# Optimization experiments

Hardware: AMD Instinct MI355X
Metric: run time of the kernel (lower is better)

## Reference

```python
import jax, jax.numpy as jnp
import numpy as np

B, T, C, H = 8, 1024, 768, 12
HD = C // H
EPS = 1e-5
NEG = jnp.finfo(jnp.float32).min


def layer_norm(x, scale, bias):
    mu = jnp.mean(x, axis=-1, keepdims=True)
    var = jnp.mean(jnp.square(x - mu), axis=-1, keepdims=True)
    return (x - mu) * jax.lax.rsqrt(var + EPS) * scale + bias


def setup_inputs() -> dict:
    key = jax.random.key(0)
    ks = jax.random.split(key, 8)
    s = lambda fan_in: 1.0 / np.sqrt(fan_in)
    x = jax.random.normal(ks[0], (B, T, C), dtype=jnp.float32)
    mask = jnp.tril(jnp.ones((T, T), dtype=bool))[None, None, :, :]
    return {
        "x": x,
        "mask": mask,
        "ln1_scale": jnp.ones((C,), jnp.float32),
        "ln1_bias": jnp.zeros((C,), jnp.float32),
        "w_qkv": jax.random.normal(ks[1], (C, 3 * C), jnp.float32) * s(C),
        "b_qkv": jnp.zeros((3 * C,), jnp.float32),
        "w_attn_proj": jax.random.normal(ks[2], (C, C), jnp.float32) * s(C),
        "b_attn_proj": jnp.zeros((C,), jnp.float32),
        "ln2_scale": jnp.ones((C,), jnp.float32),
        "ln2_bias": jnp.zeros((C,), jnp.float32),
        "w_fc": jax.random.normal(ks[3], (C, 4 * C), jnp.float32) * s(C),
        "b_fc": jnp.zeros((4 * C,), jnp.float32),
        "w_mlp_proj": jax.random.normal(ks[4], (4 * C, C), jnp.float32) * s(4 * C),
        "b_mlp_proj": jnp.zeros((C,), jnp.float32),
    }


def reference(x, mask, ln1_scale, ln1_bias, w_qkv, b_qkv, w_attn_proj,
              b_attn_proj, ln2_scale, ln2_bias, w_fc, b_fc, w_mlp_proj,
              b_mlp_proj):
    # --- attention branch (pre-LN) ---
    h = layer_norm(x, ln1_scale, ln1_bias)
    qkv = jnp.einsum('btc,cd->btd', h, w_qkv) + b_qkv      # [B,T,3C]
    qkv = qkv.reshape(B, T, 3 * H, HD)
    q, k, v = jnp.array_split(qkv, 3, axis=2)              # each [B,T,H,HD]
    scale = 1.0 / jnp.sqrt(jnp.float32(HD))
    attn = jnp.einsum('bqhd,bkhd->bhqk', q, k) * scale     # [B,H,T,T]
    attn = jnp.where(mask, attn, NEG)
    attn = jax.nn.softmax(attn, axis=-1)
    ctx = jnp.einsum('bhqk,bkhd->bqhd', attn, v).reshape(B, T, C)
    attn_out = jnp.einsum('btc,cd->btd', ctx, w_attn_proj) + b_attn_proj
    x = x + attn_out
    # --- MLP branch (pre-LN) ---
    h = layer_norm(x, ln2_scale, ln2_bias)
    h = jax.nn.gelu(jnp.einsum('btc,cf->btf', h, w_fc) + b_fc)  # tanh approx, as flax default
    mlp_out = jnp.einsum('btf,fc->btc', h, w_mlp_proj) + b_mlp_proj
    return x + mlp_out
```

## Files before the change

### kernel.cpp

```cpp
#include <hip/hip_runtime.h>
#include <hip/hip_bf16.h>
#include <cstdint>
#include <math.h>

#define BB 8
#define TT 1024
#define CC 768
#define HH 12
#define MROWS (BB*TT)

typedef __hip_bfloat16 bf16;
typedef __attribute__((ext_vector_type(8))) __bf16 bf16x8;
typedef __attribute__((ext_vector_type(4))) float f32x4;

#define MFMA16(a,b,c) __builtin_amdgcn_mfma_f32_16x16x32_bf16(a,b,c,0,0,0)

__device__ __forceinline__ void lds_barrier() {
  asm volatile("s_waitcnt lgkmcnt(0)\n\ts_barrier" ::: "memory");
}

__global__ __launch_bounds__(256) void ln_kernel(
    const float* __restrict__ x, const float* __restrict__ scale,
    const float* __restrict__ bias, bf16* __restrict__ out)
{
  int row = blockIdx.x;
  const float* xr = x + (size_t)row * CC;
  float v[3];
  float s = 0.f, s2 = 0.f;
  for (int i = 0; i < 3; i++) {
    v[i] = xr[threadIdx.x + i*256];
    s += v[i]; s2 += v[i]*v[i];
  }
  for (int m = 1; m < 64; m <<= 1) { s += __shfl_xor(s, m); s2 += __shfl_xor(s2, m); }
  __shared__ float ssum[4], ssum2[4];
  int w = threadIdx.x >> 6;
  if ((threadIdx.x & 63) == 0) { ssum[w] = s; ssum2[w] = s2; }
  __syncthreads();
  s = ssum[0]+ssum[1]+ssum[2]+ssum[3];
  s2 = ssum2[0]+ssum2[1]+ssum2[2]+ssum2[3];
  float mu = s * (1.f/CC);
  float var = s2 * (1.f/CC) - mu*mu;
  float rs = rsqrtf(var + 1e-5f);
  bf16* orow = out + (size_t)row * CC;
  for (int i = 0; i < 3; i++) {
    int c = threadIdx.x + i*256;
    orow[c] = __float2bfloat16((v[i]-mu)*rs*scale[c] + bias[c]);
  }
}

__global__ __launch_bounds__(256) void wtrans_kernel(
    const float* __restrict__ src, bf16* __restrict__ dst, int K, int N)
{
  __shared__ float tile[32][33];
  int n0 = blockIdx.x * 32, k0 = blockIdx.y * 32;
  int tx = threadIdx.x & 31, ty = threadIdx.x >> 5;
  for (int i = 0; i < 4; i++)
    tile[ty + i*8][tx] = src[(size_t)(k0 + ty + i*8)*N + n0 + tx];
  __syncthreads();
  for (int i = 0; i < 4; i++)
    dst[(size_t)(n0 + ty + i*8)*K + k0 + tx] = __float2bfloat16(tile[tx][ty + i*8]);
}

__global__ __launch_bounds__(256) void vtrans_kernel(
    const bf16* __restrict__ src, bf16* __restrict__ dst)
{
  __shared__ bf16 tile[64][65];
  int bh = blockIdx.x >> 4, t0 = (blockIdx.x & 15) * 64;
  const bf16* s = src + ((size_t)bh * TT + t0) * 64;
  for (int i = 0; i < 16; i++) {
    int idx = threadIdx.x + i*256;
    tile[idx >> 6][idx & 63] = s[idx];
  }
  __syncthreads();
  bf16* o = dst + (size_t)bh * 64 * TT + t0;
  for (int i = 0; i < 16; i++) {
    int idx = threadIdx.x + i*256;
    int d = idx >> 6, t = idx & 63;
    o[(size_t)d * TT + t] = tile[t][d];
  }
}

template<int EPI>
__global__ __launch_bounds__(256) void gemm_bt(
    const bf16* __restrict__ A, const bf16* __restrict__ Bt,
    const float* __restrict__ bias, int Mdim, int Ndim, int Kdim,
    const float* __restrict__ res, void* __restrict__ out0,
    bf16* __restrict__ outK, bf16* __restrict__ outV)
{
  __shared__ bf16 As[2][128*32];
  __shared__ bf16 Bs[2][128*32];
  int tid = threadIdx.x;
  int wave = tid >> 6, lane = tid & 63;
  int quad = lane >> 4, l15 = lane & 15;
  int wr = wave >> 1, wc = wave & 1;

  int Nb = gridDim.x;
  int lin = blockIdx.y * Nb + blockIdx.x;
  int band = lin / (8*Nb);
  int rem  = lin - band*8*Nb;
  int m0 = (band*8 + (rem & 7)) * 128;
  int n0 = (rem >> 3) * 128;

  const int sub = lane >> 2;
  const int kk = (lane & 3) * 8;

  f32x4 acc[4][4];
  for (int i = 0; i < 4; i++) for (int j = 0; j < 4; j++)
    acc[i][j] = (f32x4){0.f,0.f,0.f,0.f};

  const bf16* pa0 = A  + (size_t)(m0 + wave*16      + sub)*Kdim + kk;
  const bf16* pa1 = A  + (size_t)(m0 + (4+wave)*16  + sub)*Kdim + kk;
  const bf16* pb0 = Bt + (size_t)(n0 + wave*16      + sub)*Kdim + kk;
  const bf16* pb1 = Bt + (size_t)(n0 + (4+wave)*16  + sub)*Kdim + kk;
  const int woff0 = wave*512     + lane*8;
  const int woff1 = (4+wave)*512 + lane*8;

  const int niter = Kdim >> 5;

  bf16x8 ra0 = *reinterpret_cast<const bf16x8*>(pa0);
  bf16x8 ra1 = *reinterpret_cast<const bf16x8*>(pa1);
  bf16x8 rb0 = *reinterpret_cast<const bf16x8*>(pb0);
  bf16x8 rb1 = *reinterpret_cast<const bf16x8*>(pb1);
  pa0 += 32; pa1 += 32; pb0 += 32; pb1 += 32;
  *reinterpret_cast<bf16x8*>(As[0] + woff0) = ra0;
  *reinterpret_cast<bf16x8*>(As[0] + woff1) = ra1;
  *reinterpret_cast<bf16x8*>(Bs[0] + woff0) = rb0;
  *reinterpret_cast<bf16x8*>(Bs[0] + woff1) = rb1;
  lds_barrier();

  for (int it = 0; it < niter; it++) {
    int cur = it & 1, nxt = cur ^ 1;
    bool more = (it + 1 < niter);
    if (more) {
      ra0 = *reinterpret_cast<const bf16x8*>(pa0);
      ra1 = *reinterpret_cast<const bf16x8*>(pa1);
      rb0 = *reinterpret_cast<const bf16x8*>(pb0);
      rb1 = *reinterpret_cast<const bf16x8*>(pb1);
      pa0 += 32; pa1 += 32; pb0 += 32; pb1 += 32;
    }
    bf16x8 bfr[4];
    for (int j = 0; j < 4; j++)
      bfr[j] = *reinterpret_cast<const bf16x8*>(Bs[cur] + (wc*64 + j*16 + l15)*32 + quad*8);
    for (int i = 0; i < 4; i++) {
      bf16x8 af = *reinterpret_cast<const bf16x8*>(As[cur] + (wr*64 + i*16 + l15)*32 + quad*8);
      for (int j = 0; j < 4; j++)
        acc[i][j] = MFMA16(af, bfr[j], acc[i][j]);
    }
    if (more) {
      *reinterpret_cast<bf16x8*>(As[nxt] + woff0) = ra0;
      *reinterpret_cast<bf16x8*>(As[nxt] + woff1) = ra1;
      *reinterpret_cast<bf16x8*>(Bs[nxt] + woff0) = rb0;
      *reinterpret_cast<bf16x8*>(Bs[nxt] + woff1) = rb1;
      lds_barrier();
    }
  }

  for (int i = 0; i < 4; i++) {
    for (int j = 0; j < 4; j++) {
      for (int r = 0; r < 4; r++) {
        int row = m0 + wr*64 + i*16 + quad*4 + r;
        int col = n0 + wc*64 + j*16 + l15;
        float cv = acc[i][j][r] + bias[col];
        if (EPI == 0) {
          int part = col / 768;
          int cc = col - part*768;
          int h = cc >> 6, d = cc & 63;
          int b = row >> 10, t = row & 1023;
          bf16* dst = (part == 0) ? (bf16*)out0 : (part == 1) ? outK : outV;
          dst[(((size_t)(b*HH + h))*TT + t)*64 + d] = __float2bfloat16(cv);
        } else if (EPI == 1) {
          ((float*)out0)[(size_t)row*Ndim + col] = cv + res[(size_t)row*Ndim + col];
        } else {
          float u = cv;
          float y = 0.7978845608f*(u + 0.044715f*u*u*u);
          float e = __expf(2.f*fabsf(y));
          float z = 2.f/(e + 1.f);
          float sel = (y >= 0.f) ? (2.f - z) : z;
          ((bf16*)out0)[(size_t)row*Ndim + col] = __float2bfloat16(0.5f*u*sel);
        }
      }
    }
  }
}

__global__ __launch_bounds__(256) void attn_kernel(
    const bf16* __restrict__ Q, const bf16* __restrict__ Kb,
    const bf16* __restrict__ Vt, bf16* __restrict__ ctx)
{
  __shared__ bf16 Ks[64*64];
  __shared__ bf16 Vs[64*64];
  __shared__ bf16 Ps[4*16*64];

  int tid = threadIdx.x, wave = tid >> 6, lane = tid & 63;
  int quad = lane >> 4, l15 = lane & 15;
  int bh = blockIdx.x >> 4;
  int tile = 15 - (blockIdx.x & 15);
  int q0b = tile*64;
  int q0w = q0b + wave*16;
  int b = bh / HH, h = bh - b*HH;
  const bf16* Qp = Q + ((size_t)bh*TT + q0w)*64;
  const bf16* Kp = Kb + (size_t)bh*TT*64;
  const bf16* Vp = Vt + (size_t)bh*64*TT;
  bf16* Pw = Ps + wave*16*64;

  bf16x8 qf[2];
  qf[0] = *reinterpret_cast<const bf16x8*>(Qp + l15*64 + quad*8);
  qf[1] = *reinterpret_cast<const bf16x8*>(Qp + l15*64 + 32 + quad*8);

  f32x4 O[4];
  for (int j = 0; j < 4; j++) O[j] = (f32x4){0.f,0.f,0.f,0.f};
  float lsum[4] = {0.f, 0.f, 0.f, 0.f};
  const float c2 = 0.18033688f;

  const int srow0 = wave*16 + (lane >> 3);
  const int sc    = lane & 7;

  int nc = tile + 1;

  bf16x8 kreg[2], vreg[2], kreg2[2], vreg2[2];
  for (int rep = 0; rep < 2; rep++) {
    int row = srow0 + rep*8;
    kreg[rep] = *reinterpret_cast<const bf16x8*>(Kp + (size_t)row*64 + sc*8);
    vreg[rep] = *reinterpret_cast<const bf16x8*>(Vp + (size_t)row*TT + sc*8);
  }

  for (int ci = 0; ci < nc; ci++) {
    int kbase = ci*64;
    __syncthreads();
    for (int rep = 0; rep < 2; rep++) {
      int row = srow0 + rep*8;
      int ph = sc ^ (row & 7);
      *reinterpret_cast<bf16x8*>(Ks + row*64 + ph*8) = kreg[rep];
      *reinterpret_cast<bf16x8*>(Vs + row*64 + ph*8) = vreg[rep];
    }
    if (ci + 1 < nc) {
      int kb2 = kbase + 64;
      for (int rep = 0; rep < 2; rep++) {
        int row = srow0 + rep*8;
        kreg2[rep] = *reinterpret_cast<const bf16x8*>(Kp + (size_t)(kb2 + row)*64 + sc*8);
        vreg2[rep] = *reinterpret_cast<const bf16x8*>(Vp + (size_t)row*TT + kb2 + sc*8);
      }
    }
    __syncthreads();

    f32x4 S[4];
    for (int j = 0; j < 4; j++) S[j] = (f32x4){0.f,0.f,0.f,0.f};
    for (int kh = 0; kh < 2; kh++) {
      for (int j = 0; j < 4; j++) {
        int key = j*16 + l15;
        bf16x8 kf = *reinterpret_cast<const bf16x8*>(
            Ks + key*64 + ((kh*4 + quad) ^ (key & 7))*8);
        S[j] = MFMA16(qf[kh], kf, S[j]);
      }
    }

    float p[4][4];
    if (kbase + 63 > q0w) {
      for (int j = 0; j < 4; j++) {
        int key = kbase + j*16 + l15;
        for (int r = 0; r < 4; r++) {
          int row = q0w + quad*4 + r;
          p[j][r] = (key <= row) ? __builtin_amdgcn_exp2f(S[j][r]*c2) : 0.f;
        }
      }
    } else {
      for (int j = 0; j < 4; j++)
        for (int r = 0; r < 4; r++)
          p[j][r] = __builtin_amdgcn_exp2f(S[j][r]*c2);
    }
    for (int j = 0; j < 4; j++)
      for (int r = 0; r < 4; r++) lsum[r] += p[j][r];

    for (int j = 0; j < 4; j++) {
      int cblk = j*2 + (l15 >> 3);
      int koff = l15 & 7;
      for (int r = 0; r < 4; r++) {
        int q = quad*4 + r;
        Pw[q*64 + (cblk ^ (q & 7))*8 + koff] = __float2bfloat16(p[j][r]);
      }
    }

    for (int kh = 0; kh < 2; kh++) {
      bf16x8 pf = *reinterpret_cast<const bf16x8*>(
          Pw + l15*64 + ((kh*4 + quad) ^ (l15 & 7))*8);
      for (int j = 0; j < 4; j++) {
        int d = j*16 + l15;
        bf16x8 vf = *reinterpret_cast<const bf16x8*>(
            Vs + d*64 + ((kh*4 + quad) ^ (d & 7))*8);
        O[j] = MFMA16(pf, vf, O[j]);
      }
    }

    for (int rep = 0; rep < 2; rep++) { kreg[rep] = kreg2[rep]; vreg[rep] = vreg2[rep]; }
  }

  for (int r = 0; r < 4; r++)
    for (int msk = 1; msk < 16; msk <<= 1)
      lsum[r] += __shfl_xor(lsum[r], msk);

  bf16* cp = ctx + ((size_t)b*TT + q0w)*CC + h*64;
  for (int r = 0; r < 4; r++) {
    float inv = 1.f / lsum[r];
    int row = quad*4 + r;
    for (int j = 0; j < 4; j++)
      cp[(size_t)row*CC + j*16 + l15] = __float2bfloat16(O[j][r]*inv);
  }
}

extern "C" void kernel_launch(void* const* d_in, const int* in_sizes, int n_in,
                              void* d_out, int out_size, void* d_ws, size_t ws_size,
                              hipStream_t stream)
{
  const float* x    = (const float*)d_in[0];
  const float* ln1s = (const float*)d_in[2];
  const float* ln1b = (const float*)d_in[3];
  const float* wqkv = (const float*)d_in[4];
  const float* bqkv = (const float*)d_in[5];
  const float* wap  = (const float*)d_in[6];
  const float* bap  = (const float*)d_in[7];
  const float* ln2s = (const float*)d_in[8];
  const float* ln2b = (const float*)d_in[9];
  const float* wfc  = (const float*)d_in[10];
  const float* bfc  = (const float*)d_in[11];
  const float* wmp  = (const float*)d_in[12];
  const float* bmp  = (const float*)d_in[13];

  char* ws = (char*)d_ws;
  bf16* wqkv_t = (bf16*)ws; ws += (size_t)2304*768*2;
  bf16* wap_t  = (bf16*)ws; ws += (size_t)768*768*2;
  bf16* wfc_t  = (bf16*)ws; ws += (size_t)3072*768*2;
  bf16* wmp_t  = (bf16*)ws; ws += (size_t)768*3072*2;
  bf16* buf1   = (bf16*)ws; ws += (size_t)MROWS*CC*2;
  bf16* Qb     = (bf16*)ws; ws += (size_t)MROWS*CC*2;
  bf16* Kbuf   = (bf16*)ws; ws += (size_t)MROWS*CC*2;
  bf16* Vb     = (bf16*)ws; ws += (size_t)MROWS*CC*2;
  bf16* Vt     = (bf16*)ws; ws += (size_t)MROWS*CC*2;
  bf16* g      = Qb;
  float* r1    = (float*)ws; ws += (size_t)MROWS*CC*4;

  dim3 blk(256);
  wtrans_kernel<<<dim3(2304/32, 768/32), blk, 0, stream>>>(wqkv, wqkv_t, 768, 2304);
  wtrans_kernel<<<dim3(768/32, 768/32), blk, 0, stream>>>(wap, wap_t, 768, 768);
  wtrans_kernel<<<dim3(3072/32, 768/32), blk, 0, stream>>>(wfc, wfc_t, 768, 3072);
  wtrans_kernel<<<dim3(768/32, 3072/32), blk, 0, stream>>>(wmp, wmp_t, 3072, 768);
  ln_kernel<<<MROWS, blk, 0, stream>>>(x, ln1s, ln1b, buf1);
  gemm_bt<0><<<dim3(2304/128, MROWS/128), blk, 0, stream>>>(
      buf1, wqkv_t, bqkv, MROWS, 2304, 768, nullptr, (void*)Qb, Kbuf, Vb);
  vtrans_kernel<<<BB*HH*16, blk, 0, stream>>>(Vb, Vt);
  attn_kernel<<<BB*HH*16, blk, 0, stream>>>(Qb, Kbuf, Vt, buf1);
  gemm_bt<1><<<dim3(768/128, MROWS/128), blk, 0, stream>>>(
      buf1, wap_t, bap, MROWS, 768, 768, x, (void*)r1, nullptr, nullptr);
  ln_kernel<<<MROWS, blk, 0, stream>>>(r1, ln2s, ln2b, buf1);
  gemm_bt<2><<<dim3(3072/128, MROWS/128), blk, 0, stream>>>(
      buf1, wfc_t, bfc, MROWS, 3072, 768, nullptr, (void*)g, nullptr, nullptr);
  gemm_bt<1><<<dim3(768/128, MROWS/128), blk, 0, stream>>>(
      g, wmp_t, bmp, MROWS, 768, 3072, r1, d_out, nullptr, nullptr);
}
```

Baseline: 377.5 us.

## Add 256x256-tile GEMM with direct global-to-LDS loads for QKV and FC

Introduces a new 512-thread GEMM kernel with 256x256 output tiles, a 4-stage LDS ring fed by global_load_lds (direct-to-LDS) copies, swizzled LDS layout, and wave priority raising around MFMA blocks. It replaces the 128x128 GEMM for the QKV projection and the FC+GELU layer, aiming at more data reuse per tile and better overlap of loads with MFMA compute. The larger tiles lower block counts (288 and 384 blocks) and raise register and LDS pressure (128 KB LDS per block), which may hurt occupancy and wave balance across CUs.

```diff
diff --git a/kernel.cpp b/kernel.cpp
--- a/kernel.cpp
+++ b/kernel.cpp
@@ -17,6 +17,12 @@
 
 __device__ __forceinline__ void lds_barrier() {
   asm volatile("s_waitcnt lgkmcnt(0)\n\ts_barrier" ::: "memory");
+}
+
+typedef __attribute__((address_space(1))) const void av1;
+typedef __attribute__((address_space(3))) void av3;
+__device__ __forceinline__ void gload16(const bf16* g, bf16* l) {
+  __builtin_amdgcn_global_load_lds((av1*)g, (av3*)l, 16, 0, 0);
 }
 
 __global__ __launch_bounds__(256) void ln_kernel(
@@ -183,6 +189,136 @@
   }
 }
 
+template<int EPI>
+__global__ __launch_bounds__(512, 2) void gemm256(
+    const bf16* __restrict__ A, const bf16* __restrict__ Bt,
+    const float* __restrict__ bias, int Mdim, int Ndim, int Kdim,
+    const float* __restrict__ res, void* __restrict__ out0,
+    bf16* __restrict__ outK, bf16* __restrict__ outV)
+{
+  __shared__ bf16 sA[4*256*32];
+  __shared__ bf16 sB[4*256*32];
+
+  const int tid = threadIdx.x;
+  const int wave = tid >> 6, lane = tid & 63;
+  const int quad = lane >> 4, l15 = lane & 15;
+  const int wr = wave >> 2, wc = wave & 3;
+
+  const int m0 = blockIdx.y * 256;
+  const int n0 = blockIdx.x * 256;
+
+  const int srow  = lane >> 2;
+  const int sslot = (lane & 3) ^ ((lane >> 3) & 3);
+  const bf16* gA0 = A  + (size_t)(m0 + wave*16 + srow) * Kdim + sslot*8;
+  const bf16* gA1 = gA0 + (size_t)128 * Kdim;
+  const bf16* gB0 = Bt + (size_t)(n0 + wave*16 + srow) * Kdim + sslot*8;
+  const bf16* gB1 = gB0 + (size_t)128 * Kdim;
+  const int ldsL0 = wave*512;
+  const int ldsL1 = 4096 + wave*512;
+
+  const int sw = quad ^ ((l15 >> 1) & 3);
+  const int aoff = (wr*128 + l15)*32 + sw*8;
+  const int boff = (wc*64  + l15)*32 + sw*8;
+
+  f32x4 acc[8][4];
+  #pragma unroll
+  for (int i = 0; i < 8; i++)
+    #pragma unroll
+    for (int j = 0; j < 4; j++)
+      acc[i][j] = (f32x4){0.f,0.f,0.f,0.f};
+
+  const int NT = Kdim >> 5;
+
+  for (int t = 0; t < 3; ++t) {
+    const int b = t * 8192;
+    const size_t ko = (size_t)t * 32;
+    gload16(gA0 + ko, sA + b + ldsL0);
+    gload16(gA1 + ko, sA + b + ldsL1);
+    gload16(gB0 + ko, sB + b + ldsL0);
+    gload16(gB1 + ko, sB + b + ldsL1);
+  }
+
+  for (int t = 0; t < NT; ++t) {
+    const int bb = (t & 3) * 8192;
+    if (t + 2 < NT)
+      asm volatile("s_waitcnt vmcnt(8) lgkmcnt(0)\n\ts_barrier" ::: "memory");
+    else if (t + 1 < NT)
+      asm volatile("s_waitcnt vmcnt(4) lgkmcnt(0)\n\ts_barrier" ::: "memory");
+    else
+      asm volatile("s_waitcnt vmcnt(0) lgkmcnt(0)\n\ts_barrier" ::: "memory");
+
+    bf16x8 bfr[4], afr[4];
+    #pragma unroll
+    for (int j = 0; j < 4; j++)
+      bfr[j] = *reinterpret_cast<const bf16x8*>(sB + bb + boff + j*512);
+    #pragma unroll
+    for (int i = 0; i < 4; i++)
+      afr[i] = *reinterpret_cast<const bf16x8*>(sA + bb + aoff + i*512);
+
+    if (t + 3 < NT) {
+      const int b3 = ((t+3) & 3) * 8192;
+      const size_t ko = (size_t)(t+3) * 32;
+      gload16(gA0 + ko, sA + b3 + ldsL0);
+      gload16(gA1 + ko, sA + b3 + ldsL1);
+    }
+    __builtin_amdgcn_s_setprio(1);
+    #pragma unroll
+    for (int i = 0; i < 4; i++)
+      #pragma unroll
+      for (int j = 0; j < 4; j++)
+        acc[i][j] = MFMA16(afr[i], bfr[j], acc[i][j]);
+    __builtin_amdgcn_s_setprio(0);
+
+    #pragma unroll
+    for (int i = 0; i < 4; i++)
+      afr[i] = *reinterpret_cast<const bf16x8*>(sA + bb + aoff + 2048 + i*512);
+
+    if (t + 3 < NT) {
+      const int b3 = ((t+3) & 3) * 8192;
+      const size_t ko = (size_t)(t+3) * 32;
+      gload16(gB0 + ko, sB + b3 + ldsL0);
+      gload16(gB1 + ko, sB + b3 + ldsL1);
+    }
+    __builtin_amdgcn_s_setprio(1);
+    #pragma unroll
+    for (int i = 0; i < 4; i++)
+      #pragma unroll
+      for (int j = 0; j < 4; j++)
+        acc[i+4][j] = MFMA16(afr[i], bfr[j], acc[i+4][j]);
+    __builtin_amdgcn_s_setprio(0);
+  }
+
+  #pragma unroll
+  for (int i = 0; i < 8; i++) {
+    #pragma unroll
+    for (int j = 0; j < 4; j++) {
+      #pragma unroll
+      for (int r = 0; r < 4; r++) {
+        int row = m0 + wr*128 + i*16 + quad*4 + r;
+        int col = n0 + wc*64 + j*16 + l15;
+        float cv = acc[i][j][r] + bias[col];
+        if (EPI == 0) {
+          int part = col / 768;
+          int cc = col - part*768;
+          int h = cc >> 6, d = cc & 63;
+          int b = row >> 10, t = row & 1023;
+          bf16* dst = (part == 0) ? (bf16*)out0 : (part == 1) ? outK : outV;
+          dst[(((size_t)(b*HH + h))*TT + t)*64 + d] = __float2bfloat16(cv);
+        } else if (EPI == 1) {
+          ((float*)out0)[(size_t)row*Ndim + col] = cv + res[(size_t)row*Ndim + col];
+        } else {
+          float u = cv;
+          float y = 0.7978845608f*(u + 0.044715f*u*u*u);
+          float e = __expf(2.f*fabsf(y));
+          float z = 2.f/(e + 1.f);
+          float sel = (y >= 0.f) ? (2.f - z) : z;
+          ((bf16*)out0)[(size_t)row*Ndim + col] = __float2bfloat16(0.5f*u*sel);
+        }
+      }
+    }
+  }
+}
+
 __global__ __launch_bounds__(256) void attn_kernel(
     const bf16* __restrict__ Q, const bf16* __restrict__ Kb,
     const bf16* __restrict__ Vt, bf16* __restrict__ ctx)
@@ -344,14 +480,14 @@
   wtrans_kernel<<<dim3(3072/32, 768/32), blk, 0, stream>>>(wfc, wfc_t, 768, 3072);
   wtrans_kernel<<<dim3(768/32, 3072/32), blk, 0, stream>>>(wmp, wmp_t, 3072, 768);
   ln_kernel<<<MROWS, blk, 0, stream>>>(x, ln1s, ln1b, buf1);
-  gemm_bt<0><<<dim3(2304/128, MROWS/128), blk, 0, stream>>>(
+  gemm256<0><<<dim3(2304/256, MROWS/256), dim3(512), 0, stream>>>(
       buf1, wqkv_t, bqkv, MROWS, 2304, 768, nullptr, (void*)Qb, Kbuf, Vb);
   vtrans_kernel<<<BB*HH*16, blk, 0, stream>>>(Vb, Vt);
   attn_kernel<<<BB*HH*16, blk, 0, stream>>>(Qb, Kbuf, Vt, buf1);
   gemm_bt<1><<<dim3(768/128, MROWS/128), blk, 0, stream>>>(
       buf1, wap_t, bap, MROWS, 768, 768, x, (void*)r1, nullptr, nullptr);
   ln_kernel<<<MROWS, blk, 0, stream>>>(r1, ln2s, ln2b, buf1);
-  gemm_bt<2><<<dim3(3072/128, MROWS/128), blk, 0, stream>>>(
+  gemm256<2><<<dim3(3072/256, MROWS/256), dim3(512), 0, stream>>>(
       buf1, wfc_t, bfc, MROWS, 3072, 768, nullptr, (void*)g, nullptr, nullptr);
   gemm_bt<1><<<dim3(768/128, MROWS/128), blk, 0, stream>>>(
       g, wmp_t, bmp, MROWS, 768, 3072, r1, d_out, nullptr, nullptr);
```

Result: slower. 397.3 us (+5.2%).
